# Kernel tuning notes

Hardware: AMD Instinct MI355X
Metric: run time of the kernel (lower is better)

The kernel has to match this reference:

```python
import jax, jax.numpy as jnp
import numpy as np

N = 100000   # nodes
E = 1200000  # edges
G = 128      # graphs in batch
VOCAB = 10000
D = 64       # node_emb_dim
H = 64       # hidden_dim
R = 64       # readout_dim
BN_EPS = 1e-5


def _mlp_bn(h, W1, b1, g, be, W2, b2):
    # PyG MLP([in,H,H], act='ELU'): Linear -> BatchNorm(eval, running mean=0, var=1) -> ELU -> Linear
    h = h @ W1 + b1
    h = h * (g / jnp.sqrt(1.0 + BN_EPS)) + be
    h = jax.nn.elu(h)
    return h @ W2 + b2


def _gin(h, src, dst, W1, b1, g, be, W2, b2):
    # GINConv(eps=0): nn((1+0)*x_i + sum_{j->i} x_j)
    agg = jax.ops.segment_sum(h[src], dst, num_segments=N)
    return _mlp_bn(h + agg, W1, b1, g, be, W2, b2)


def setup_inputs() -> dict:
    key = jax.random.key(0)
    ks = iter(jax.random.split(key, 40))
    inp = {}
    inp["x"] = jax.random.randint(next(ks), (N, 1), 0, VOCAB)
    inp["edge_index"] = jax.random.randint(next(ks), (2, E), 0, N)
    inp["batch"] = jnp.sort(jax.random.randint(next(ks), (N,), 0, G))
    # embedding init: normal with std = dim**-0.5 (matches initialize_parameters)
    inp["emb"] = jax.random.normal(next(ks), (VOCAB, D), jnp.float32) * (D ** -0.5)

    def lin(k, fi, fo):
        return jax.random.normal(k, (fi, fo), jnp.float32) / np.sqrt(fi)

    for tag, fi in (("a", D), ("b", H), ("c", H)):
        inp[f"W1{tag}"] = lin(next(ks), fi, H)
        inp[f"b1{tag}"] = jnp.zeros((H,), jnp.float32)
        inp[f"g{tag}"] = jnp.ones((H,), jnp.float32)
        inp[f"be{tag}"] = jnp.zeros((H,), jnp.float32)
        inp[f"W2{tag}"] = lin(next(ks), H, H)
        inp[f"b2{tag}"] = jnp.zeros((H,), jnp.float32)

    inp["Wr1"] = lin(next(ks), H, H)
    inp["br1"] = jnp.zeros((H,), jnp.float32)
    inp["Wr2"] = lin(next(ks), H, R)
    inp["br2"] = jnp.zeros((R,), jnp.float32)
    inp["Wo"] = lin(next(ks), R, 1)
    inp["bo"] = jnp.zeros((1,), jnp.float32)
    return inp


def reference(x, edge_index, batch, emb,
              W1a, b1a, ga, bea, W2a, b2a,
              W1b, b1b, gb, beb, W2b, b2b,
              W1c, b1c, gc, bec, W2c, b2c,
              Wr1, br1, Wr2, br2, Wo, bo):
    # eval mode: dropout layers are identity
    src, dst = edge_index[0], edge_index[1]
    h = emb[x[:, 0]]                                        # [N, D]
    h = jax.nn.elu(_gin(h, src, dst, W1a, b1a, ga, bea, W2a, b2a))
    h = jax.nn.elu(_gin(h, src, dst, W1b, b1b, gb, beb, W2b, b2b))
    h = jax.nn.elu(_gin(h, src, dst, W1c, b1c, gc, bec, W2c, b2c))
    # global mean pool over graphs
    sums = jax.ops.segment_sum(h, batch, num_segments=G)    # [G, H]
    cnts = jax.ops.segment_sum(jnp.ones((N,), h.dtype), batch, num_segments=G)
    pooled = sums / jnp.maximum(cnts, 1.0)[:, None]
    # readout MLP (norm=None, dropout inactive in eval): Lin -> ELU -> Lin
    r = jax.nn.elu(pooled @ Wr1 + br1) @ Wr2 + br2
    return r @ Wo + bo                                      # [G, 1]
```

## Files before the change

### kernel.cpp

```cpp
#include <hip/hip_runtime.h>
#include <hip/hip_bf16.h>

#define N_NODES 100000
#define N_EDGES 1200000
#define G_GRAPHS 128
#define CAP 64
#define AP 68
#define SLICE_N 12500

__global__ void scatter_k(const int* __restrict__ ei, int* __restrict__ cnt,
                          int* __restrict__ adj) {
    int slice = blockIdx.x & 7;
    int e = (blockIdx.x >> 3) * 256 + threadIdx.x;
    if (e >= N_EDGES) return;
    int s = ei[e];
    int d = ei[N_EDGES + e];
    s = min(max(s, 0), N_NODES - 1);
    d = min(max(d, 0), N_NODES - 1);
    if (d / SLICE_N != slice) return;
    int pos = atomicAdd(&cnt[d], 1);
    if (pos < CAP) adj[d * CAP + pos] = s;
}

__global__ void embed_k(const int* __restrict__ x, const float4* __restrict__ emb,
                        float4* __restrict__ h) {
    int t = blockIdx.x * 256 + threadIdx.x;
    if (t >= N_NODES * 16) return;
    int n = t >> 4, q = t & 15;
    h[n * 16 + q] = emb[x[n] * 16 + q];
}

__device__ __forceinline__ void f4add(float4& a, const float4 b) {
    a.x += b.x; a.y += b.y; a.z += b.z; a.w += b.w;
}

__device__ __forceinline__ float elu(float v) { return v > 0.f ? v : expm1f(v); }

#define FMA16(comp, wv)                                                        \
    acc[0][0] += av0.comp * wv.x; acc[0][1] += av0.comp * wv.y;                \
    acc[0][2] += av0.comp * wv.z; acc[0][3] += av0.comp * wv.w;                \
    acc[1][0] += av1.comp * wv.x; acc[1][1] += av1.comp * wv.y;                \
    acc[1][2] += av1.comp * wv.z; acc[1][3] += av1.comp * wv.w;                \
    acc[2][0] += av2.comp * wv.x; acc[2][1] += av2.comp * wv.y;                \
    acc[2][2] += av2.comp * wv.z; acc[2][3] += av2.comp * wv.w;                \
    acc[3][0] += av3.comp * wv.x; acc[3][1] += av3.comp * wv.y;                \
    acc[3][2] += av3.comp * wv.z; acc[3][3] += av3.comp * wv.w;

__device__ __forceinline__ void mm64(const float* __restrict__ A,
                                     const float* __restrict__ Ws,
                                     float acc[4][4], int tr, int tc) {
    #pragma unroll 2
    for (int k4 = 0; k4 < 16; ++k4) {
        float4 av0 = *(const float4*)(A + (tr * 4 + 0) * AP + k4 * 4);
        float4 av1 = *(const float4*)(A + (tr * 4 + 1) * AP + k4 * 4);
        float4 av2 = *(const float4*)(A + (tr * 4 + 2) * AP + k4 * 4);
        float4 av3 = *(const float4*)(A + (tr * 4 + 3) * AP + k4 * 4);
        {
            float4 wv = *(const float4*)(Ws + (k4 * 4 + 0) * 64 + tc * 4);
            FMA16(x, wv)
        }
        {
            float4 wv = *(const float4*)(Ws + (k4 * 4 + 1) * 64 + tc * 4);
            FMA16(y, wv)
        }
        {
            float4 wv = *(const float4*)(Ws + (k4 * 4 + 2) * 64 + tc * 4);
            FMA16(z, wv)
        }
        {
            float4 wv = *(const float4*)(Ws + (k4 * 4 + 3) * 64 + tc * 4);
            FMA16(w, wv)
        }
    }
}

__global__ void __launch_bounds__(256, 4) mlp_k(const float* __restrict__ hin,
    float* __restrict__ hout, const int* __restrict__ adj,
    const int* __restrict__ cnt,
    const float* __restrict__ W1, const float* __restrict__ b1,
    const float* __restrict__ g,  const float* __restrict__ be,
    const float* __restrict__ W2, const float* __restrict__ b2) {
    __shared__ float At[64 * AP];
    __shared__ float Wbuf[4096];
    __shared__ float sc1[64], ep1[64], ep2[64];
    int tid = threadIdx.x;
    int n0 = blockIdx.x * 64;
    const float4* h4 = (const float4*)hin;

    for (int idx = tid; idx < 1024; idx += 256)
        ((float4*)Wbuf)[idx] = ((const float4*)W1)[idx];
    if (tid < 64) {
        const float inv = rsqrtf(1.0f + 1e-5f);
        float s = g[tid] * inv;
        sc1[tid] = s;
        ep1[tid] = b1[tid] * s + be[tid];
        ep2[tid] = b2[tid];
    }
    {
        int r = tid >> 4, q = tid & 15;
        #pragma unroll
        for (int p = 0; p < 4; ++p) {
            int rr = p * 16 + r;
            int n = n0 + rr;
            float4 a0 = make_float4(0.f, 0.f, 0.f, 0.f);
            if (n < N_NODES) {
                a0 = h4[n * 16 + q];
                int deg = min(cnt[n], CAP);
                const int4* al4 = (const int4*)(adj + n * CAP);
                float4 a1 = make_float4(0.f, 0.f, 0.f, 0.f);
                float4 a2 = a1, a3 = a1, a4 = a1, a5 = a1, a6 = a1, a7 = a1;
                int g8 = (deg + 7) >> 3;
                for (int i = 0; i < g8; ++i) {
                    int4 sa = al4[2 * i];
                    int4 sb = al4[2 * i + 1];
                    int base = i * 8;
                    int s0 = (base + 0 < deg) ? sa.x : N_NODES;
                    int s1 = (base + 1 < deg) ? sa.y : N_NODES;
                    int s2 = (base + 2 < deg) ? sa.z : N_NODES;
                    int s3 = (base + 3 < deg) ? sa.w : N_NODES;
                    int s4 = (base + 4 < deg) ? sb.x : N_NODES;
                    int s5 = (base + 5 < deg) ? sb.y : N_NODES;
                    int s6 = (base + 6 < deg) ? sb.z : N_NODES;
                    int s7 = (base + 7 < deg) ? sb.w : N_NODES;
                    float4 v0 = h4[s0 * 16 + q];
                    float4 v1 = h4[s1 * 16 + q];
                    float4 v2 = h4[s2 * 16 + q];
                    float4 v3 = h4[s3 * 16 + q];
                    float4 v4 = h4[s4 * 16 + q];
                    float4 v5 = h4[s5 * 16 + q];
                    float4 v6 = h4[s6 * 16 + q];
                    float4 v7 = h4[s7 * 16 + q];
                    f4add(a0, v0); f4add(a1, v1); f4add(a2, v2); f4add(a3, v3);
                    f4add(a4, v4); f4add(a5, v5); f4add(a6, v6); f4add(a7, v7);
                }
                f4add(a0, a1); f4add(a2, a3); f4add(a4, a5); f4add(a6, a7);
                f4add(a0, a2); f4add(a4, a6); f4add(a0, a4);
            }
            *(float4*)(At + rr * AP + q * 4) = a0;
        }
    }
    __syncthreads();

    int tr = tid >> 4, tc = tid & 15;
    float acc[4][4];
    #pragma unroll
    for (int e = 0; e < 4; ++e)
        #pragma unroll
        for (int j = 0; j < 4; ++j) acc[e][j] = 0.f;

    mm64(At, Wbuf, acc, tr, tc);
    __syncthreads();
    #pragma unroll
    for (int e = 0; e < 4; ++e) {
        float4 o;
        o.x = elu(acc[e][0] * sc1[tc * 4 + 0] + ep1[tc * 4 + 0]);
        o.y = elu(acc[e][1] * sc1[tc * 4 + 1] + ep1[tc * 4 + 1]);
        o.z = elu(acc[e][2] * sc1[tc * 4 + 2] + ep1[tc * 4 + 2]);
        o.w = elu(acc[e][3] * sc1[tc * 4 + 3] + ep1[tc * 4 + 3]);
        *(float4*)(At + (tr * 4 + e) * AP + tc * 4) = o;
    }
    for (int idx = tid; idx < 1024; idx += 256)
        ((float4*)Wbuf)[idx] = ((const float4*)W2)[idx];
    __syncthreads();
    #pragma unroll
    for (int e = 0; e < 4; ++e)
        #pragma unroll
        for (int j = 0; j < 4; ++j) acc[e][j] = 0.f;

    mm64(At, Wbuf, acc, tr, tc);
    #pragma unroll
    for (int e = 0; e < 4; ++e) {
        int n = n0 + tr * 4 + e;
        if (n < N_NODES) {
            float4 o;
            o.x = elu(acc[e][0] + ep2[tc * 4 + 0]);
            o.y = elu(acc[e][1] + ep2[tc * 4 + 1]);
            o.z = elu(acc[e][2] + ep2[tc * 4 + 2]);
            o.w = elu(acc[e][3] + ep2[tc * 4 + 3]);
            ((float4*)hout)[n * 16 + tc] = o;
        }
    }
}

__global__ void pool_k(const float4* __restrict__ h, const int* __restrict__ batch,
                       float4* __restrict__ pooled) {
    int gph = blockIdx.x;
    int tid = threadIdx.x;
    int lo = 0, hi = N_NODES;
    while (lo < hi) { int mid = (lo + hi) >> 1; if (batch[mid] < gph) lo = mid + 1; else hi = mid; }
    int start = lo;
    hi = N_NODES;
    while (lo < hi) { int mid = (lo + hi) >> 1; if (batch[mid] < gph + 1) lo = mid + 1; else hi = mid; }
    int end = lo;
    int q = tid & 15, r = tid >> 4;
    float4 acc = make_float4(0.f, 0.f, 0.f, 0.f);
    for (int n = start + r; n < end; n += 16) {
        float4 v = h[n * 16 + q];
        acc.x += v.x; acc.y += v.y; acc.z += v.z; acc.w += v.w;
    }
    __shared__ float4 red[256];
    red[tid] = acc;
    __syncthreads();
    for (int s = 8; s > 0; s >>= 1) {
        if (r < s) {
            float4 o = red[(r + s) * 16 + q];
            float4 m = red[r * 16 + q];
            m.x += o.x; m.y += o.y; m.z += o.z; m.w += o.w;
            red[r * 16 + q] = m;
        }
        __syncthreads();
    }
    if (r == 0) {
        float invc = 1.0f / fmaxf((float)(end - start), 1.0f);
        float4 m = red[q];
        m.x *= invc; m.y *= invc; m.z *= invc; m.w *= invc;
        pooled[gph * 16 + q] = m;
    }
}

__global__ void __launch_bounds__(256) head_k(const float* __restrict__ pooled,
    const float* __restrict__ Wr1, const float* __restrict__ br1,
    const float* __restrict__ Wr2, const float* __restrict__ br2,
    const float* __restrict__ Wo,  const float* __restrict__ bo,
    float* __restrict__ out) {
    __shared__ float ylds[4][64];
    int wid = threadIdx.x >> 6, j = threadIdx.x & 63;
    int gph = blockIdx.x * 4 + wid;
    float acc = 0.f;
    #pragma unroll 8
    for (int k = 0; k < 64; ++k)
        acc += pooled[gph * 64 + k] * Wr1[k * 64 + j];
    float yv = acc + br1[j];
    ylds[wid][j] = elu(yv);
    __syncthreads();
    float acc2 = 0.f;
    #pragma unroll 8
    for (int k = 0; k < 64; ++k)
        acc2 += ylds[wid][k] * Wr2[k * 64 + j];
    float p = (acc2 + br2[j]) * Wo[j];
    #pragma unroll
    for (int off = 32; off > 0; off >>= 1) p += __shfl_down(p, off);
    if (j == 0) out[gph] = bo[0] + p;
}

extern "C" void kernel_launch(void* const* d_in, const int* in_sizes, int n_in,
                              void* d_out, int out_size, void* d_ws, size_t ws_size,
                              hipStream_t stream) {
    const int*   x     = (const int*)d_in[0];
    const int*   ei    = (const int*)d_in[1];
    const int*   batch = (const int*)d_in[2];
    const float* emb   = (const float*)d_in[3];
    const float* P[24];
    for (int i = 0; i < 24; ++i) P[i] = (const float*)d_in[4 + i];

    char* ws = (char*)d_ws;
    float* hA     = (float*)(ws + 0);
    float* hB     = (float*)(ws + 26000000);
    int*   adj    = (int*)  (ws + 52000000);
    int*   cnt    = (int*)  (ws + 78000000);
    float* pooled = (float*)(ws + 78400000);

    hipMemsetAsync(cnt, 0, N_NODES * sizeof(int), stream);
    hipMemsetAsync(hA + N_NODES * 64, 0, 64 * sizeof(float), stream);
    hipMemsetAsync(hB + N_NODES * 64, 0, 64 * sizeof(float), stream);
    scatter_k<<<8 * ((N_EDGES + 255) / 256), 256, 0, stream>>>(ei, cnt, adj);
    embed_k<<<(N_NODES * 16 + 255) / 256, 256, 0, stream>>>(x, (const float4*)emb, (float4*)hA);
    for (int L = 0; L < 3; ++L) {
        const float* const* p = P + 6 * L;
        const float* hin = (L & 1) ? hB : hA;
        float* hout      = (L & 1) ? hA : hB;
        mlp_k<<<(N_NODES + 63) / 64, 256, 0, stream>>>(
            hin, hout, adj, cnt, p[0], p[1], p[2], p[3], p[4], p[5]);
    }
    pool_k<<<G_GRAPHS, 256, 0, stream>>>((const float4*)hB, batch, (float4*)pooled);
    head_k<<<32, 256, 0, stream>>>(pooled, P[18], P[19], P[20], P[21], P[22], P[23],
                                   (float*)d_out);
}
```

Baseline: 419.2 us.

## Store node features in bf16 to halve gather traffic

Node feature buffers between GIN layers are stored as bf16 (round-to-nearest-even), and values are unpacked to fp32 when gathered, aggregated and pooled. The edge gather, which dominates the kernel, reads half as many bytes per neighbor row, so the feature table is also more likely to stay in cache. The memsets are folded into the embedding kernel, which now zeroes the counters and the padding rows. The cost is precision loss in intermediate activations and possible tolerance risk.

```diff
diff --git a/kernel.cpp b/kernel.cpp
--- a/kernel.cpp
+++ b/kernel.cpp
@@ -7,6 +7,22 @@
 #define CAP 64
 #define AP 68
 #define SLICE_N 12500
+
+__device__ __forceinline__ ushort f2bf(float f) {
+    uint u = __float_as_uint(f);
+    return (ushort)((u + 0x7FFF + ((u >> 16) & 1)) >> 16);
+}
+__device__ __forceinline__ uint pack2(float a, float b) {
+    return (uint)f2bf(a) | ((uint)f2bf(b) << 16);
+}
+__device__ __forceinline__ float4 bf4(uint2 w) {
+    float4 r;
+    r.x = __uint_as_float(w.x << 16);
+    r.y = __uint_as_float(w.x & 0xFFFF0000u);
+    r.z = __uint_as_float(w.y << 16);
+    r.w = __uint_as_float(w.y & 0xFFFF0000u);
+    return r;
+}
 
 __global__ void scatter_k(const int* __restrict__ ei, int* __restrict__ cnt,
                           int* __restrict__ adj) {
@@ -23,11 +39,19 @@
 }
 
 __global__ void embed_k(const int* __restrict__ x, const float4* __restrict__ emb,
-                        float4* __restrict__ h) {
+                        ushort* __restrict__ hbfA, ushort* __restrict__ hbfB,
+                        int* __restrict__ cnt) {
     int t = blockIdx.x * 256 + threadIdx.x;
-    if (t >= N_NODES * 16) return;
+    if (t > N_NODES * 16 + 15) return;
     int n = t >> 4, q = t & 15;
-    h[n * 16 + q] = emb[x[n] * 16 + q];
+    if (t < N_NODES) cnt[t] = 0;
+    if (n < N_NODES) {
+        float4 v = emb[x[n] * 16 + q];
+        *(uint2*)(hbfA + n * 64 + q * 4) = make_uint2(pack2(v.x, v.y), pack2(v.z, v.w));
+    } else {
+        *(uint2*)(hbfA + n * 64 + q * 4) = make_uint2(0u, 0u);
+        *(uint2*)(hbfB + n * 64 + q * 4) = make_uint2(0u, 0u);
+    }
 }
 
 __device__ __forceinline__ void f4add(float4& a, const float4 b) {
@@ -74,8 +98,8 @@
     }
 }
 
-__global__ void __launch_bounds__(256, 4) mlp_k(const float* __restrict__ hin,
-    float* __restrict__ hout, const int* __restrict__ adj,
+__global__ void __launch_bounds__(256, 4) mlp_k(const ushort* __restrict__ hin,
+    ushort* __restrict__ hout, const int* __restrict__ adj,
     const int* __restrict__ cnt,
     const float* __restrict__ W1, const float* __restrict__ b1,
     const float* __restrict__ g,  const float* __restrict__ be,
@@ -85,7 +109,6 @@
     __shared__ float sc1[64], ep1[64], ep2[64];
     int tid = threadIdx.x;
     int n0 = blockIdx.x * 64;
-    const float4* h4 = (const float4*)hin;
 
     for (int idx = tid; idx < 1024; idx += 256)
         ((float4*)Wbuf)[idx] = ((const float4*)W1)[idx];
@@ -104,7 +127,7 @@
             int n = n0 + rr;
             float4 a0 = make_float4(0.f, 0.f, 0.f, 0.f);
             if (n < N_NODES) {
-                a0 = h4[n * 16 + q];
+                a0 = bf4(*(const uint2*)(hin + n * 64 + q * 4));
                 int deg = min(cnt[n], CAP);
                 const int4* al4 = (const int4*)(adj + n * CAP);
                 float4 a1 = make_float4(0.f, 0.f, 0.f, 0.f);
@@ -122,16 +145,18 @@
                     int s5 = (base + 5 < deg) ? sb.y : N_NODES;
                     int s6 = (base + 6 < deg) ? sb.z : N_NODES;
                     int s7 = (base + 7 < deg) ? sb.w : N_NODES;
-                    float4 v0 = h4[s0 * 16 + q];
-                    float4 v1 = h4[s1 * 16 + q];
-                    float4 v2 = h4[s2 * 16 + q];
-                    float4 v3 = h4[s3 * 16 + q];
-                    float4 v4 = h4[s4 * 16 + q];
-                    float4 v5 = h4[s5 * 16 + q];
-                    float4 v6 = h4[s6 * 16 + q];
-                    float4 v7 = h4[s7 * 16 + q];
-                    f4add(a0, v0); f4add(a1, v1); f4add(a2, v2); f4add(a3, v3);
-                    f4add(a4, v4); f4add(a5, v5); f4add(a6, v6); f4add(a7, v7);
+                    uint2 w0 = *(const uint2*)(hin + s0 * 64 + q * 4);
+                    uint2 w1 = *(const uint2*)(hin + s1 * 64 + q * 4);
+                    uint2 w2 = *(const uint2*)(hin + s2 * 64 + q * 4);
+                    uint2 w3 = *(const uint2*)(hin + s3 * 64 + q * 4);
+                    uint2 w4 = *(const uint2*)(hin + s4 * 64 + q * 4);
+                    uint2 w5 = *(const uint2*)(hin + s5 * 64 + q * 4);
+                    uint2 w6 = *(const uint2*)(hin + s6 * 64 + q * 4);
+                    uint2 w7 = *(const uint2*)(hin + s7 * 64 + q * 4);
+                    f4add(a0, bf4(w0)); f4add(a1, bf4(w1));
+                    f4add(a2, bf4(w2)); f4add(a3, bf4(w3));
+                    f4add(a4, bf4(w4)); f4add(a5, bf4(w5));
+                    f4add(a6, bf4(w6)); f4add(a7, bf4(w7));
                 }
                 f4add(a0, a1); f4add(a2, a3); f4add(a4, a5); f4add(a6, a7);
                 f4add(a0, a2); f4add(a4, a6); f4add(a0, a4);
@@ -172,17 +197,16 @@
     for (int e = 0; e < 4; ++e) {
         int n = n0 + tr * 4 + e;
         if (n < N_NODES) {
-            float4 o;
-            o.x = elu(acc[e][0] + ep2[tc * 4 + 0]);
-            o.y = elu(acc[e][1] + ep2[tc * 4 + 1]);
-            o.z = elu(acc[e][2] + ep2[tc * 4 + 2]);
-            o.w = elu(acc[e][3] + ep2[tc * 4 + 3]);
-            ((float4*)hout)[n * 16 + tc] = o;
-        }
-    }
-}
-
-__global__ void pool_k(const float4* __restrict__ h, const int* __restrict__ batch,
+            float o0 = elu(acc[e][0] + ep2[tc * 4 + 0]);
+            float o1 = elu(acc[e][1] + ep2[tc * 4 + 1]);
+            float o2 = elu(acc[e][2] + ep2[tc * 4 + 2]);
+            float o3 = elu(acc[e][3] + ep2[tc * 4 + 3]);
+            *(uint2*)(hout + n * 64 + tc * 4) = make_uint2(pack2(o0, o1), pack2(o2, o3));
+        }
+    }
+}
+
+__global__ void pool_k(const ushort* __restrict__ h, const int* __restrict__ batch,
                        float4* __restrict__ pooled) {
     int gph = blockIdx.x;
     int tid = threadIdx.x;
@@ -194,10 +218,8 @@
     int end = lo;
     int q = tid & 15, r = tid >> 4;
     float4 acc = make_float4(0.f, 0.f, 0.f, 0.f);
-    for (int n = start + r; n < end; n += 16) {
-        float4 v = h[n * 16 + q];
-        acc.x += v.x; acc.y += v.y; acc.z += v.z; acc.w += v.w;
-    }
+    for (int n = start + r; n < end; n += 16)
+        f4add(acc, bf4(*(const uint2*)(h + n * 64 + q * 4)));
     __shared__ float4 red[256];
     red[tid] = acc;
     __syncthreads();
@@ -254,25 +276,23 @@
     for (int i = 0; i < 24; ++i) P[i] = (const float*)d_in[4 + i];
 
     char* ws = (char*)d_ws;
-    float* hA     = (float*)(ws + 0);
-    float* hB     = (float*)(ws + 26000000);
-    int*   adj    = (int*)  (ws + 52000000);
-    int*   cnt    = (int*)  (ws + 78000000);
-    float* pooled = (float*)(ws + 78400000);
-
-    hipMemsetAsync(cnt, 0, N_NODES * sizeof(int), stream);
-    hipMemsetAsync(hA + N_NODES * 64, 0, 64 * sizeof(float), stream);
-    hipMemsetAsync(hB + N_NODES * 64, 0, 64 * sizeof(float), stream);
+    ushort* hbfA  = (ushort*)(ws + 0);
+    ushort* hbfB  = (ushort*)(ws + 13000000);
+    int*    adj   = (int*)   (ws + 26000000);
+    int*    cnt   = (int*)   (ws + 52000000);
+    float*  pooled= (float*) (ws + 52500000);
+
+    embed_k<<<(N_NODES * 16 + 16 + 255) / 256, 256, 0, stream>>>(
+        x, (const float4*)emb, hbfA, hbfB, cnt);
     scatter_k<<<8 * ((N_EDGES + 255) / 256), 256, 0, stream>>>(ei, cnt, adj);
-    embed_k<<<(N_NODES * 16 + 255) / 256, 256, 0, stream>>>(x, (const float4*)emb, (float4*)hA);
     for (int L = 0; L < 3; ++L) {
         const float* const* p = P + 6 * L;
-        const float* hin = (L & 1) ? hB : hA;
-        float* hout      = (L & 1) ? hA : hB;
+        const ushort* hin = (L & 1) ? hbfB : hbfA;
+        ushort* hout      = (L & 1) ? hbfA : hbfB;
         mlp_k<<<(N_NODES + 63) / 64, 256, 0, stream>>>(
             hin, hout, adj, cnt, p[0], p[1], p[2], p[3], p[4], p[5]);
     }
-    pool_k<<<G_GRAPHS, 256, 0, stream>>>((const float4*)hB, batch, (float4*)pooled);
+    pool_k<<<G_GRAPHS, 256, 0, stream>>>(hbfB, batch, (float4*)pooled);
     head_k<<<32, 256, 0, stream>>>(pooled, P[18], P[19], P[20], P[21], P[22], P[23],
                                    (float*)d_out);
 }
```

Measured after the change: 371.3 us. 1.13x faster.
